# Kernel optimization log

Measured on AMD Instinct MI355X. Metric: run time of the kernel, lower is better.

Reference implementation:

```python
import jax, jax.numpy as jnp
import numpy as np

D_MODEL = 2048
NUM_EXPERTS = 64
TOP_K = 2
N_TOKENS = 16384


def setup_inputs() -> dict:
    key = jax.random.key(0)
    kx, kw = jax.random.split(key)
    x = jax.random.normal(kx, (N_TOKENS, D_MODEL), dtype=jnp.float32)
    # match nn.Linear default init scale roughly (not bit-exact; math is what matters)
    W = jax.random.normal(kw, (D_MODEL, NUM_EXPERTS), dtype=jnp.float32) * (1.0 / np.sqrt(D_MODEL))
    b = jnp.zeros((NUM_EXPERTS,), dtype=jnp.float32)
    return {"x": x, "W": W, "b": b}


def reference(x, W, b):
    # eval-mode forward (self.training False => no noise)
    logits = jnp.einsum("td,de->te", x, W) + b          # [T, E]
    weights = jax.nn.softmax(logits, axis=-1)             # [T, E]
    topk_weights, topk_indices = jax.lax.top_k(weights, TOP_K)  # [T, k] each
    return topk_weights, topk_indices, weights
```

## Files before the change

### kernel.cpp

```cpp
#include <hip/hip_runtime.h>
#include <math.h>


#define T_TOK 16384
#define DMOD 2048
#define NEXP 64
#define TM 64
#define BK 32
#define NT 256
#define NCHUNK (DMOD / BK)

__global__ __launch_bounds__(NT) void gating_kernel(
    const float* __restrict__ x, const float* __restrict__ W,
    const float* __restrict__ bias, float* __restrict__ out) {
  __shared__ float xs[2][BK][TM];
  __shared__ float ws[2][BK][NEXP];
  __shared__ float lg[TM][NEXP + 1];
  __shared__ float red_m[TM];
  __shared__ float red_s[TM];

  const int tid = threadIdx.x;
  const int t0 = blockIdx.x * TM;
  const int ty = tid >> 4;
  const int tx = tid & 15;
  const int st_t = tid & 63;
  const int st_c = tid >> 6;

  float acc[4][4];
#pragma unroll
  for (int i = 0; i < 4; ++i)
#pragma unroll
    for (int e = 0; e < 4; ++e) acc[i][e] = 0.f;

  const float* xg = x + (size_t)(t0 + st_t) * DMOD + st_c * 4;
  const float* wg = W + tid * 4;

  {
    const float4 a  = *(const float4*)(xg);
    const float4 b  = *(const float4*)(xg + 16);
    const float4 wa = *(const float4*)(wg);
    const float4 wb = *(const float4*)(wg + 1024);
    const int d0 = st_c * 4;
    xs[0][d0 + 0][st_t] = a.x;  xs[0][d0 + 1][st_t] = a.y;
    xs[0][d0 + 2][st_t] = a.z;  xs[0][d0 + 3][st_t] = a.w;
    xs[0][16 + d0 + 0][st_t] = b.x;  xs[0][16 + d0 + 1][st_t] = b.y;
    xs[0][16 + d0 + 2][st_t] = b.z;  xs[0][16 + d0 + 3][st_t] = b.w;
    *(float4*)(&ws[0][0][0] + tid * 4) = wa;
    *(float4*)(&ws[0][0][0] + 1024 + tid * 4) = wb;
  }
  __syncthreads();

  int buf = 0;
  for (int k = 0; k < NCHUNK; ++k) {
    float4 pa, pb, pwa, pwb;
    const bool has_next = (k + 1 < NCHUNK);
    if (has_next) {
      const int kd = (k + 1) * BK;
      pa  = *(const float4*)(xg + kd);
      pb  = *(const float4*)(xg + kd + 16);
      pwa = *(const float4*)(wg + (size_t)kd * NEXP);
      pwb = *(const float4*)(wg + (size_t)kd * NEXP + 1024);
    }
#pragma unroll
    for (int j = 0; j < BK; ++j) {
      const float4 xv = *(const float4*)&xs[buf][j][ty * 4];
      const float4 wv = *(const float4*)&ws[buf][j][tx * 4];
      acc[0][0] = fmaf(xv.x, wv.x, acc[0][0]);
      acc[0][1] = fmaf(xv.x, wv.y, acc[0][1]);
      acc[0][2] = fmaf(xv.x, wv.z, acc[0][2]);
      acc[0][3] = fmaf(xv.x, wv.w, acc[0][3]);
      acc[1][0] = fmaf(xv.y, wv.x, acc[1][0]);
      acc[1][1] = fmaf(xv.y, wv.y, acc[1][1]);
      acc[1][2] = fmaf(xv.y, wv.z, acc[1][2]);
      acc[1][3] = fmaf(xv.y, wv.w, acc[1][3]);
      acc[2][0] = fmaf(xv.z, wv.x, acc[2][0]);
      acc[2][1] = fmaf(xv.z, wv.y, acc[2][1]);
      acc[2][2] = fmaf(xv.z, wv.z, acc[2][2]);
      acc[2][3] = fmaf(xv.z, wv.w, acc[2][3]);
      acc[3][0] = fmaf(xv.w, wv.x, acc[3][0]);
      acc[3][1] = fmaf(xv.w, wv.y, acc[3][1]);
      acc[3][2] = fmaf(xv.w, wv.z, acc[3][2]);
      acc[3][3] = fmaf(xv.w, wv.w, acc[3][3]);
    }
    if (has_next) {
      const int nb = buf ^ 1;
      const int d0 = st_c * 4;
      xs[nb][d0 + 0][st_t] = pa.x;  xs[nb][d0 + 1][st_t] = pa.y;
      xs[nb][d0 + 2][st_t] = pa.z;  xs[nb][d0 + 3][st_t] = pa.w;
      xs[nb][16 + d0 + 0][st_t] = pb.x;  xs[nb][16 + d0 + 1][st_t] = pb.y;
      xs[nb][16 + d0 + 2][st_t] = pb.z;  xs[nb][16 + d0 + 3][st_t] = pb.w;
      *(float4*)(&ws[nb][0][0] + tid * 4) = pwa;
      *(float4*)(&ws[nb][0][0] + 1024 + tid * 4) = pwb;
    }
    __syncthreads();
    buf ^= 1;
  }

#pragma unroll
  for (int i = 0; i < 4; ++i)
#pragma unroll
    for (int e = 0; e < 4; ++e)
      lg[ty * 4 + i][tx * 4 + e] = acc[i][e] + bias[tx * 4 + e];
  __syncthreads();

  if (tid < TM) {
    float m = -INFINITY;
    for (int e = 0; e < NEXP; ++e) m = fmaxf(m, lg[tid][e]);
    float s = 0.f, b1 = -INFINITY, b2 = -INFINITY;
    int i1 = 0, i2 = 0;
    for (int e = 0; e < NEXP; ++e) {
      const float v = lg[tid][e];
      s += expf(v - m);
      if (v > b1) {
        b2 = b1; i2 = i1; b1 = v; i1 = e;
      } else if (v > b2) {
        b2 = v; i2 = e;
      }
    }
    const float inv = 1.f / s;
    const int t = t0 + tid;
    out[2 * t + 0] = expf(b1 - m) * inv;
    out[2 * t + 1] = expf(b2 - m) * inv;
    out[2 * T_TOK + 2 * t + 0] = (float)i1;
    out[2 * T_TOK + 2 * t + 1] = (float)i2;
    red_m[tid] = m;
    red_s[tid] = inv;
  }
  __syncthreads();

#pragma unroll
  for (int r = 0; r < (TM * NEXP) / NT; ++r) {
    const int idx = r * NT + tid;
    const int tt = idx >> 6;
    const int e = idx & 63;
    out[4 * T_TOK + (size_t)(t0 + tt) * NEXP + e] =
        expf(lg[tt][e] - red_m[tt]) * red_s[tt];
  }
}

extern "C" void kernel_launch(void* const* d_in, const int* in_sizes, int n_in,
                              void* d_out, int out_size, void* d_ws, size_t ws_size,
                              hipStream_t stream) {
  const float* x = (const float*)d_in[0];
  const float* W = (const float*)d_in[1];
  const float* b = (const float*)d_in[2];
  float* out = (float*)d_out;
  gating_kernel<<<dim3(T_TOK / TM), dim3(NT), 0, stream>>>(x, W, b, out);
}
```

Measured before the change: 232.0 us.

## Split K dimension across four thread slices with shared-memory logit reduction

Raises the block to 512 threads and splits the 2048-wide reduction into four slices, each handled by 128 threads with its own staging tiles. Each thread now computes an 8x4 output tile instead of 4x4. The partial logits are summed serially into a shared logit array before the softmax and top-k. Double buffering is replaced by a single buffer with two barriers per chunk, which adds synchronisation and shared memory (64KB) and may reduce occupancy in exchange for more parallelism per block.

New measurement: 765.0 us. +229.7%, slower.

```diff
diff --git a/kernel.cpp b/kernel.cpp
--- a/kernel.cpp
+++ b/kernel.cpp
@@ -3,121 +3,167 @@
 
 
 #define T_TOK 16384
-#define DMOD 2048
-#define NEXP 64
-#define TM 64
-#define BK 32
-#define NT 256
-#define NCHUNK (DMOD / BK)
+#define DMOD  2048
+#define NEXP  64
+#define TM    64
+#define NSL   4
+#define DSL   (DMOD / NSL)
+#define BK    32
+#define NCH   (DSL / BK)
+#define NT    512
 
 __global__ __launch_bounds__(NT) void gating_kernel(
     const float* __restrict__ x, const float* __restrict__ W,
     const float* __restrict__ bias, float* __restrict__ out) {
-  __shared__ float xs[2][BK][TM];
-  __shared__ float ws[2][BK][NEXP];
-  __shared__ float lg[TM][NEXP + 1];
-  __shared__ float red_m[TM];
-  __shared__ float red_s[TM];
+  __shared__ float smem[16384];
+  float* xs = smem;
+  float* ws = smem + 8192;
+  float* lg = smem;
+  float* red_m = smem + 4160;
+  float* red_s = smem + 4224;
 
-  const int tid = threadIdx.x;
-  const int t0 = blockIdx.x * TM;
-  const int ty = tid >> 4;
-  const int tx = tid & 15;
-  const int st_t = tid & 63;
-  const int st_c = tid >> 6;
+  const int tid  = threadIdx.x;
+  const int s    = tid >> 7;
+  const int sl   = tid & 127;
+  const int tg   = sl >> 4;
+  const int eg   = sl & 15;
+  const int tt   = sl >> 1;
+  const int half = sl & 1;
+  const int t0   = blockIdx.x * TM;
 
-  float acc[4][4];
+  const float* xg = x + (size_t)(t0 + tt) * DMOD + s * DSL + half * 16;
+  const float* wg = W + (size_t)(s * DSL) * NEXP;
+  float* xs_s = xs + s * 2048;
+  float* ws_s = ws + s * 2048;
+
+  float acc[8][4];
 #pragma unroll
-  for (int i = 0; i < 4; ++i)
+  for (int i = 0; i < 8; ++i)
 #pragma unroll
     for (int e = 0; e < 4; ++e) acc[i][e] = 0.f;
 
-  const float* xg = x + (size_t)(t0 + st_t) * DMOD + st_c * 4;
-  const float* wg = W + tid * 4;
-
   {
-    const float4 a  = *(const float4*)(xg);
-    const float4 b  = *(const float4*)(xg + 16);
-    const float4 wa = *(const float4*)(wg);
-    const float4 wb = *(const float4*)(wg + 1024);
-    const int d0 = st_c * 4;
-    xs[0][d0 + 0][st_t] = a.x;  xs[0][d0 + 1][st_t] = a.y;
-    xs[0][d0 + 2][st_t] = a.z;  xs[0][d0 + 3][st_t] = a.w;
-    xs[0][16 + d0 + 0][st_t] = b.x;  xs[0][16 + d0 + 1][st_t] = b.y;
-    xs[0][16 + d0 + 2][st_t] = b.z;  xs[0][16 + d0 + 3][st_t] = b.w;
-    *(float4*)(&ws[0][0][0] + tid * 4) = wa;
-    *(float4*)(&ws[0][0][0] + 1024 + tid * 4) = wb;
+    float4 px[4], pw[4];
+#pragma unroll
+    for (int r = 0; r < 4; ++r) px[r] = *(const float4*)(xg + r * 4);
+#pragma unroll
+    for (int r = 0; r < 4; ++r) pw[r] = ((const float4*)wg)[r * 128 + sl];
+#pragma unroll
+    for (int r = 0; r < 4; ++r) {
+      const int d = half * 16 + r * 4;
+      xs_s[(d + 0) * 64 + tt] = px[r].x;
+      xs_s[(d + 1) * 64 + tt] = px[r].y;
+      xs_s[(d + 2) * 64 + tt] = px[r].z;
+      xs_s[(d + 3) * 64 + tt] = px[r].w;
+      ((float4*)ws_s)[r * 128 + sl] = pw[r];
+    }
   }
   __syncthreads();
 
-  int buf = 0;
-  for (int k = 0; k < NCHUNK; ++k) {
-    float4 pa, pb, pwa, pwb;
-    const bool has_next = (k + 1 < NCHUNK);
-    if (has_next) {
+  for (int k = 0; k < NCH; ++k) {
+    float4 px[4], pw[4];
+    const bool nx = (k + 1 < NCH);
+    if (nx) {
       const int kd = (k + 1) * BK;
-      pa  = *(const float4*)(xg + kd);
-      pb  = *(const float4*)(xg + kd + 16);
-      pwa = *(const float4*)(wg + (size_t)kd * NEXP);
-      pwb = *(const float4*)(wg + (size_t)kd * NEXP + 1024);
+#pragma unroll
+      for (int r = 0; r < 4; ++r) px[r] = *(const float4*)(xg + kd + r * 4);
+#pragma unroll
+      for (int r = 0; r < 4; ++r)
+        pw[r] = ((const float4*)(wg + (size_t)kd * NEXP))[r * 128 + sl];
     }
 #pragma unroll
     for (int j = 0; j < BK; ++j) {
-      const float4 xv = *(const float4*)&xs[buf][j][ty * 4];
-      const float4 wv = *(const float4*)&ws[buf][j][tx * 4];
-      acc[0][0] = fmaf(xv.x, wv.x, acc[0][0]);
-      acc[0][1] = fmaf(xv.x, wv.y, acc[0][1]);
-      acc[0][2] = fmaf(xv.x, wv.z, acc[0][2]);
-      acc[0][3] = fmaf(xv.x, wv.w, acc[0][3]);
-      acc[1][0] = fmaf(xv.y, wv.x, acc[1][0]);
-      acc[1][1] = fmaf(xv.y, wv.y, acc[1][1]);
-      acc[1][2] = fmaf(xv.y, wv.z, acc[1][2]);
-      acc[1][3] = fmaf(xv.y, wv.w, acc[1][3]);
-      acc[2][0] = fmaf(xv.z, wv.x, acc[2][0]);
-      acc[2][1] = fmaf(xv.z, wv.y, acc[2][1]);
-      acc[2][2] = fmaf(xv.z, wv.z, acc[2][2]);
-      acc[2][3] = fmaf(xv.z, wv.w, acc[2][3]);
-      acc[3][0] = fmaf(xv.w, wv.x, acc[3][0]);
-      acc[3][1] = fmaf(xv.w, wv.y, acc[3][1]);
-      acc[3][2] = fmaf(xv.w, wv.z, acc[3][2]);
-      acc[3][3] = fmaf(xv.w, wv.w, acc[3][3]);
-    }
-    if (has_next) {
-      const int nb = buf ^ 1;
-      const int d0 = st_c * 4;
-      xs[nb][d0 + 0][st_t] = pa.x;  xs[nb][d0 + 1][st_t] = pa.y;
-      xs[nb][d0 + 2][st_t] = pa.z;  xs[nb][d0 + 3][st_t] = pa.w;
-      xs[nb][16 + d0 + 0][st_t] = pb.x;  xs[nb][16 + d0 + 1][st_t] = pb.y;
-      xs[nb][16 + d0 + 2][st_t] = pb.z;  xs[nb][16 + d0 + 3][st_t] = pb.w;
-      *(float4*)(&ws[nb][0][0] + tid * 4) = pwa;
-      *(float4*)(&ws[nb][0][0] + 1024 + tid * 4) = pwb;
+      const float4 xa = *(const float4*)(xs_s + j * 64 + tg * 8);
+      const float4 xb = *(const float4*)(xs_s + j * 64 + tg * 8 + 4);
+      const float4 wv = *(const float4*)(ws_s + j * 64 + eg * 4);
+      acc[0][0] = fmaf(xa.x, wv.x, acc[0][0]);
+      acc[0][1] = fmaf(xa.x, wv.y, acc[0][1]);
+      acc[0][2] = fmaf(xa.x, wv.z, acc[0][2]);
+      acc[0][3] = fmaf(xa.x, wv.w, acc[0][3]);
+      acc[1][0] = fmaf(xa.y, wv.x, acc[1][0]);
+      acc[1][1] = fmaf(xa.y, wv.y, acc[1][1]);
+      acc[1][2] = fmaf(xa.y, wv.z, acc[1][2]);
+      acc[1][3] = fmaf(xa.y, wv.w, acc[1][3]);
+      acc[2][0] = fmaf(xa.z, wv.x, acc[2][0]);
+      acc[2][1] = fmaf(xa.z, wv.y, acc[2][1]);
+      acc[2][2] = fmaf(xa.z, wv.z, acc[2][2]);
+      acc[2][3] = fmaf(xa.z, wv.w, acc[2][3]);
+      acc[3][0] = fmaf(xa.w, wv.x, acc[3][0]);
+      acc[3][1] = fmaf(xa.w, wv.y, acc[3][1]);
+      acc[3][2] = fmaf(xa.w, wv.z, acc[3][2]);
+      acc[3][3] = fmaf(xa.w, wv.w, acc[3][3]);
+      acc[4][0] = fmaf(xb.x, wv.x, acc[4][0]);
+      acc[4][1] = fmaf(xb.x, wv.y, acc[4][1]);
+      acc[4][2] = fmaf(xb.x, wv.z, acc[4][2]);
+      acc[4][3] = fmaf(xb.x, wv.w, acc[4][3]);
+      acc[5][0] = fmaf(xb.y, wv.x, acc[5][0]);
+      acc[5][1] = fmaf(xb.y, wv.y, acc[5][1]);
+      acc[5][2] = fmaf(xb.y, wv.z, acc[5][2]);
+      acc[5][3] = fmaf(xb.y, wv.w, acc[5][3]);
+      acc[6][0] = fmaf(xb.z, wv.x, acc[6][0]);
+      acc[6][1] = fmaf(xb.z, wv.y, acc[6][1]);
+      acc[6][2] = fmaf(xb.z, wv.z, acc[6][2]);
+      acc[6][3] = fmaf(xb.z, wv.w, acc[6][3]);
+      acc[7][0] = fmaf(xb.w, wv.x, acc[7][0]);
+      acc[7][1] = fmaf(xb.w, wv.y, acc[7][1]);
+      acc[7][2] = fmaf(xb.w, wv.z, acc[7][2]);
+      acc[7][3] = fmaf(xb.w, wv.w, acc[7][3]);
     }
     __syncthreads();
-    buf ^= 1;
+    if (nx) {
+#pragma unroll
+      for (int r = 0; r < 4; ++r) {
+        const int d = half * 16 + r * 4;
+        xs_s[(d + 0) * 64 + tt] = px[r].x;
+        xs_s[(d + 1) * 64 + tt] = px[r].y;
+        xs_s[(d + 2) * 64 + tt] = px[r].z;
+        xs_s[(d + 3) * 64 + tt] = px[r].w;
+        ((float4*)ws_s)[r * 128 + sl] = pw[r];
+      }
+    }
+    __syncthreads();
   }
 
+  {
+    const float4 bv = *(const float4*)(bias + eg * 4);
 #pragma unroll
-  for (int i = 0; i < 4; ++i)
+    for (int ss = 0; ss < NSL; ++ss) {
+      if (s == ss) {
 #pragma unroll
-    for (int e = 0; e < 4; ++e)
-      lg[ty * 4 + i][tx * 4 + e] = acc[i][e] + bias[tx * 4 + e];
-  __syncthreads();
+        for (int i = 0; i < 8; ++i) {
+          float* lrow = lg + (tg * 8 + i) * 65 + eg * 4;
+          if (ss == 0) {
+            lrow[0] = acc[i][0] + bv.x;
+            lrow[1] = acc[i][1] + bv.y;
+            lrow[2] = acc[i][2] + bv.z;
+            lrow[3] = acc[i][3] + bv.w;
+          } else {
+            lrow[0] += acc[i][0];
+            lrow[1] += acc[i][1];
+            lrow[2] += acc[i][2];
+            lrow[3] += acc[i][3];
+          }
+        }
+      }
+      __syncthreads();
+    }
+  }
 
   if (tid < TM) {
     float m = -INFINITY;
-    for (int e = 0; e < NEXP; ++e) m = fmaxf(m, lg[tid][e]);
-    float s = 0.f, b1 = -INFINITY, b2 = -INFINITY;
+    for (int e = 0; e < NEXP; ++e) m = fmaxf(m, lg[tid * 65 + e]);
+    float sum = 0.f, b1 = -INFINITY, b2 = -INFINITY;
     int i1 = 0, i2 = 0;
     for (int e = 0; e < NEXP; ++e) {
-      const float v = lg[tid][e];
-      s += expf(v - m);
+      const float v = lg[tid * 65 + e];
+      sum += expf(v - m);
       if (v > b1) {
         b2 = b1; i2 = i1; b1 = v; i1 = e;
       } else if (v > b2) {
         b2 = v; i2 = e;
       }
     }
-    const float inv = 1.f / s;
+    const float inv = 1.f / sum;
     const int t = t0 + tid;
     out[2 * t + 0] = expf(b1 - m) * inv;
     out[2 * t + 1] = expf(b2 - m) * inv;
@@ -131,10 +177,10 @@
 #pragma unroll
   for (int r = 0; r < (TM * NEXP) / NT; ++r) {
     const int idx = r * NT + tid;
-    const int tt = idx >> 6;
+    const int ttk = idx >> 6;
     const int e = idx & 63;
-    out[4 * T_TOK + (size_t)(t0 + tt) * NEXP + e] =
-        expf(lg[tt][e] - red_m[tt]) * red_s[tt];
+    out[4 * T_TOK + (size_t)(t0 + ttk) * NEXP + e] =
+        expf(lg[ttk * 65 + e] - red_m[ttk]) * red_s[ttk];
   }
 }
 
```
